# Kernel optimization log

Measured on AMD Instinct MI355X. Metric: run time of the kernel, lower is better.

Reference implementation:

```python
import jax, jax.numpy as jnp
import numpy as np

BATCH = 8192
N = 32
A_NUM = 5
EPS = 1e-10
ALPHA = jnp.array([0.01, 0.25, 0.5, 0.9, 0.99], dtype=jnp.float32)


def setup_inputs() -> dict:
    key = jax.random.key(0)
    ks = jax.random.split(key, 9)
    stdv = 1.0 / np.sqrt(N)
    u = lambda k, shape: jax.random.uniform(k, shape, jnp.float32, -stdv, stdv)
    L = N * (N - 1) // 2
    return {
        "inputs": jax.random.normal(ks[0], (BATCH, N, N), jnp.float32),
        "state": jax.random.normal(ks[1], (BATCH, A_NUM * N * N), jnp.float32),
        "WR_root": u(ks[2], (A_NUM,)),
        "Wt_root": u(ks[3], (1,)),
        "Wphi_root": u(ks[4], (1,)),
        "Ws_root": u(ks[5], (A_NUM,)),
        "Br": u(ks[6], (L, 1)),
        "Bt": u(ks[7], (L, 1)),
        "By": u(ks[8], (L, 1)),
    }


def _skew(Bvec, n):
    # Replicates the torch loop: row 0 is zeros; row k (k>=1) gets B[k-1 : 2k-1]
    # in its first k columns (overlapping slices of the flat parameter vector).
    b = Bvec.reshape(-1)
    r = jnp.arange(n)[:, None]
    c = jnp.arange(n)[None, :]
    idx = jnp.clip(r - 1 + c, 0, b.shape[0] - 1)  # B[k-1+j] for entry (k, j)
    L = jnp.where(c < r, b[idx], jnp.zeros((), b.dtype))
    return L - L.T


def _cayley(S, n):
    # MatrixExp in the source: (I - S)^{-1} (I + S)
    I = jnp.eye(n, dtype=S.dtype)
    return jnp.linalg.solve(I - S, I + S)


def _translate(A, Bvec, n):
    # M @ A @ M.T with M the Cayley 'exp' of the skew matrix built from Bvec.
    M = _cayley(_skew(Bvec, n), n)
    return jnp.einsum('ij,bjk,lk->bil', M, A, M)


def _nus(W_root, A, eps):
    # Weighted average over the a_num axis with weights W_root^2 / (sum + eps).
    W = W_root * W_root
    return jnp.einsum('a,banm->bnm', W / (W.sum() + eps), A)


def reference(inputs, state, WR_root, Wt_root, Wphi_root, Ws_root, Br, Bt, By):
    Mt_1 = state.reshape(-1, A_NUM, N, N)                 # [B, a, n, n]
    X = inputs.reshape(BATCH, N, N)                       # [B, n, n]

    Yt = _nus(WR_root, Mt_1, EPS)                         # [B, n, n]
    Rt = _translate(Yt, Br, N)

    at = (Wt_root[0] ** 2) / ((Wt_root ** 2 + Wphi_root ** 2).sum() + EPS)
    Tt = (1.0 - at) * X + at * Rt                         # Frechet mean FM
    Phit = _translate(Tt, Bt, N)

    # Per-j Frechet means, vectorized over the a_num axis.
    a = ALPHA[None, :, None, None]
    Mt = (1.0 - a) * Mt_1 + a * Phit[:, None, :, :]       # [B, a, n, n]

    St = _nus(Ws_root, Mt, EPS)
    Ot = _translate(St, By, N)                            # [B, n, n]

    return Ot, Mt.reshape(-1, A_NUM, N, N)
```

## Files before the change

### kernel.cpp

```cpp
#include <hip/hip_runtime.h>

#define NB 8192
#define ANUM 5
#define OT_ELEMS (NB * 1024)
#define EPSF 1e-10f

#define WAVE_FENCE() asm volatile("s_waitcnt lgkmcnt(0)" ::: "memory")

__global__ void cayley_kernel(const float* __restrict__ Br,
                              const float* __restrict__ Bt,
                              const float* __restrict__ By,
                              float* __restrict__ MT_out) {
  __shared__ float A[32][33];
  __shared__ float R[32][33];
  const float* B = (blockIdx.x == 0) ? Br : (blockIdx.x == 1) ? Bt : By;
  const int t = threadIdx.x;
  const int i = t >> 5, j = t & 31;
  float Lij = (j < i) ? B[i - 1 + j] : 0.0f;
  float Lji = (i < j) ? B[j - 1 + i] : 0.0f;
  float S = Lij - Lji;
  float eye = (i == j) ? 1.0f : 0.0f;
  A[i][j] = eye - S;
  R[i][j] = eye + S;
  __syncthreads();
  for (int p = 0; p < 32; ++p) {
    float f = A[i][p] / A[p][p];
    __syncthreads();
    if (i != p) {
      A[i][j] -= f * A[p][j];
      R[i][j] -= f * R[p][j];
    }
    __syncthreads();
  }
  MT_out[blockIdx.x * 1024 + j * 32 + i] = R[i][j] / A[i][i];
}

__device__ __forceinline__ void mm_MQ(const float* __restrict__ M, const float* __restrict__ buf,
                                      int i0, int j0, float acc[4][4]) {
#pragma unroll
  for (int k = 0; k < 32; ++k) {
    const float4 a = *(const float4*)(M + k * 32 + i0);
    const float4 b = *(const float4*)(buf + k * 32 + (j0 ^ (k & 28)));
    acc[0][0] = fmaf(a.x, b.x, acc[0][0]);
    acc[0][1] = fmaf(a.x, b.y, acc[0][1]);
    acc[0][2] = fmaf(a.x, b.z, acc[0][2]);
    acc[0][3] = fmaf(a.x, b.w, acc[0][3]);
    acc[1][0] = fmaf(a.y, b.x, acc[1][0]);
    acc[1][1] = fmaf(a.y, b.y, acc[1][1]);
    acc[1][2] = fmaf(a.y, b.z, acc[1][2]);
    acc[1][3] = fmaf(a.y, b.w, acc[1][3]);
    acc[2][0] = fmaf(a.z, b.x, acc[2][0]);
    acc[2][1] = fmaf(a.z, b.y, acc[2][1]);
    acc[2][2] = fmaf(a.z, b.z, acc[2][2]);
    acc[2][3] = fmaf(a.z, b.w, acc[2][3]);
    acc[3][0] = fmaf(a.w, b.x, acc[3][0]);
    acc[3][1] = fmaf(a.w, b.y, acc[3][1]);
    acc[3][2] = fmaf(a.w, b.z, acc[3][2]);
    acc[3][3] = fmaf(a.w, b.w, acc[3][3]);
  }
}

__device__ __forceinline__ void mm_PM(const float* __restrict__ buf, const float* __restrict__ M,
                                      int i0, int j0, float acc[4][4]) {
#pragma unroll
  for (int k = 0; k < 32; ++k) {
    const float4 a = *(const float4*)(buf + k * 32 + (i0 ^ (k & 28)));
    const float4 b = *(const float4*)(M + k * 32 + j0);
    acc[0][0] = fmaf(a.x, b.x, acc[0][0]);
    acc[0][1] = fmaf(a.x, b.y, acc[0][1]);
    acc[0][2] = fmaf(a.x, b.z, acc[0][2]);
    acc[0][3] = fmaf(a.x, b.w, acc[0][3]);
    acc[1][0] = fmaf(a.y, b.x, acc[1][0]);
    acc[1][1] = fmaf(a.y, b.y, acc[1][1]);
    acc[1][2] = fmaf(a.y, b.z, acc[1][2]);
    acc[1][3] = fmaf(a.y, b.w, acc[1][3]);
    acc[2][0] = fmaf(a.z, b.x, acc[2][0]);
    acc[2][1] = fmaf(a.z, b.y, acc[2][1]);
    acc[2][2] = fmaf(a.z, b.z, acc[2][2]);
    acc[2][3] = fmaf(a.z, b.w, acc[2][3]);
    acc[3][0] = fmaf(a.w, b.x, acc[3][0]);
    acc[3][1] = fmaf(a.w, b.y, acc[3][1]);
    acc[3][2] = fmaf(a.w, b.z, acc[3][2]);
    acc[3][3] = fmaf(a.w, b.w, acc[3][3]);
  }
}

__global__ __launch_bounds__(256) void spdsru_main(
    const float* __restrict__ X, const float* __restrict__ state,
    const float* __restrict__ WR, const float* __restrict__ Wt,
    const float* __restrict__ Wphi, const float* __restrict__ Ws,
    const float* __restrict__ MT, float* __restrict__ out) {
  __shared__ float sMT[3 * 1024];
  __shared__ float sBuf[4][1024];
  const int t = threadIdx.x;
  for (int idx = t; idx < 768; idx += 256)
    ((float4*)sMT)[idx] = ((const float4*)MT)[idx];

  float wr[5], wsn[5];
  float sR = 0.f, sS = 0.f;
#pragma unroll
  for (int a = 0; a < 5; ++a) { float v = WR[a]; wr[a] = v * v; sR += v * v; }
#pragma unroll
  for (int a = 0; a < 5; ++a) { float v = Ws[a]; wsn[a] = v * v; sS += v * v; }
  const float invR = 1.0f / (sR + EPSF), invS = 1.0f / (sS + EPSF);
#pragma unroll
  for (int a = 0; a < 5; ++a) { wr[a] *= invR; wsn[a] *= invS; }
  const float wt2 = Wt[0] * Wt[0], wp2 = Wphi[0] * Wphi[0];
  const float at = wt2 / (wt2 + wp2 + EPSF);
  const float omat = 1.0f - at;

  const int wave = t >> 6, lane = t & 63;
  const int i0 = (lane >> 3) << 2;
  const int j0 = (lane & 7) << 2;
  const int batch = blockIdx.x * 4 + wave;
  float* buf = sBuf[wave];
  const float* MR  = sMT;
  const float* MTt = sMT + 1024;
  const float* MY  = sMT + 2048;

  const float* stp = state + (size_t)batch * (ANUM * 1024);
  const float* xp = X + (size_t)batch * 1024;
  float4 m[5][4];
#pragma unroll
  for (int a = 0; a < 5; ++a)
#pragma unroll
    for (int r = 0; r < 4; ++r)
      m[a][r] = *(const float4*)(stp + a * 1024 + (i0 + r) * 32 + j0);
  float4 x[4];
#pragma unroll
  for (int r = 0; r < 4; ++r) x[r] = *(const float4*)(xp + (i0 + r) * 32 + j0);

  __syncthreads();

#pragma unroll
  for (int r = 0; r < 4; ++r) {
    float4 y;
    y.x = wr[0]*m[0][r].x + wr[1]*m[1][r].x + wr[2]*m[2][r].x + wr[3]*m[3][r].x + wr[4]*m[4][r].x;
    y.y = wr[0]*m[0][r].y + wr[1]*m[1][r].y + wr[2]*m[2][r].y + wr[3]*m[3][r].y + wr[4]*m[4][r].y;
    y.z = wr[0]*m[0][r].z + wr[1]*m[1][r].z + wr[2]*m[2][r].z + wr[3]*m[3][r].z + wr[4]*m[4][r].z;
    y.w = wr[0]*m[0][r].w + wr[1]*m[1][r].w + wr[2]*m[2][r].w + wr[3]*m[3][r].w + wr[4]*m[4][r].w;
    *(float4*)(buf + (i0 + r) * 32 + (j0 ^ i0)) = y;
  }
  WAVE_FENCE();

  float t1[4][4] = {};
  mm_MQ(MR, buf, i0, j0, t1);
  WAVE_FENCE();
#pragma unroll
  for (int c = 0; c < 4; ++c)
    *(float4*)(buf + (j0 + c) * 32 + (i0 ^ j0)) = make_float4(t1[0][c], t1[1][c], t1[2][c], t1[3][c]);
  WAVE_FENCE();

  float t2[4][4] = {};
  mm_PM(buf, MR, i0, j0, t2);
  WAVE_FENCE();
#pragma unroll
  for (int r = 0; r < 4; ++r) {
    float4 v;
    v.x = omat * x[r].x + at * t2[r][0];
    v.y = omat * x[r].y + at * t2[r][1];
    v.z = omat * x[r].z + at * t2[r][2];
    v.w = omat * x[r].w + at * t2[r][3];
    *(float4*)(buf + (i0 + r) * 32 + (j0 ^ i0)) = v;
  }
  WAVE_FENCE();

  float u1[4][4] = {};
  mm_MQ(MTt, buf, i0, j0, u1);
  WAVE_FENCE();
#pragma unroll
  for (int c = 0; c < 4; ++c)
    *(float4*)(buf + (j0 + c) * 32 + (i0 ^ j0)) = make_float4(u1[0][c], u1[1][c], u1[2][c], u1[3][c]);
  WAVE_FENCE();

  float u2[4][4] = {};
  mm_PM(buf, MTt, i0, j0, u2);
  WAVE_FENCE();

  float* outMt = out + OT_ELEMS + (size_t)batch * (ANUM * 1024);
  float4 stl[4];
#pragma unroll
  for (int r = 0; r < 4; ++r) stl[r] = make_float4(0.f, 0.f, 0.f, 0.f);
  const float alpha[5] = {0.01f, 0.25f, 0.5f, 0.9f, 0.99f};
#pragma unroll
  for (int a = 0; a < 5; ++a) {
    const float al = alpha[a], om = 1.0f - al;
#pragma unroll
    for (int r = 0; r < 4; ++r) {
      float4 v;
      v.x = om * m[a][r].x + al * u2[r][0];
      v.y = om * m[a][r].y + al * u2[r][1];
      v.z = om * m[a][r].z + al * u2[r][2];
      v.w = om * m[a][r].w + al * u2[r][3];
      *(float4*)(outMt + a * 1024 + (i0 + r) * 32 + j0) = v;
      stl[r].x = fmaf(wsn[a], v.x, stl[r].x);
      stl[r].y = fmaf(wsn[a], v.y, stl[r].y);
      stl[r].z = fmaf(wsn[a], v.z, stl[r].z);
      stl[r].w = fmaf(wsn[a], v.w, stl[r].w);
    }
  }
#pragma unroll
  for (int r = 0; r < 4; ++r)
    *(float4*)(buf + (i0 + r) * 32 + (j0 ^ i0)) = stl[r];
  WAVE_FENCE();

  float v1[4][4] = {};
  mm_MQ(MY, buf, i0, j0, v1);
  WAVE_FENCE();
#pragma unroll
  for (int c = 0; c < 4; ++c)
    *(float4*)(buf + (j0 + c) * 32 + (i0 ^ j0)) = make_float4(v1[0][c], v1[1][c], v1[2][c], v1[3][c]);
  WAVE_FENCE();

  float v2[4][4] = {};
  mm_PM(buf, MY, i0, j0, v2);
  float* outOt = out + (size_t)batch * 1024;
#pragma unroll
  for (int r = 0; r < 4; ++r)
    *(float4*)(outOt + (i0 + r) * 32 + j0) = make_float4(v2[r][0], v2[r][1], v2[r][2], v2[r][3]);
}

extern "C" void kernel_launch(void* const* d_in, const int* in_sizes, int n_in,
                              void* d_out, int out_size, void* d_ws, size_t ws_size,
                              hipStream_t stream) {
  const float* X     = (const float*)d_in[0];
  const float* state = (const float*)d_in[1];
  const float* WR    = (const float*)d_in[2];
  const float* Wt    = (const float*)d_in[3];
  const float* Wphi  = (const float*)d_in[4];
  const float* Ws    = (const float*)d_in[5];
  const float* Br    = (const float*)d_in[6];
  const float* Bt    = (const float*)d_in[7];
  const float* By    = (const float*)d_in[8];
  float* mt_ws = (float*)d_ws;
  float* outp = (float*)d_out;

  cayley_kernel<<<3, 1024, 0, stream>>>(Br, Bt, By, mt_ws);
  spdsru_main<<<NB / 4, 256, 0, stream>>>(X, state, WR, Wt, Wphi, Ws, mt_ws, outp);
}
```

Measured before the change: 108.1 us.

## Fold state into two accumulators and reload state to cut register pressure

Instead of keeping all 80 state floats in registers across the six matmuls, the kernel reduces the state once into two weighted sums: U for the WR mix and V for the (1-alpha)-weighted Ws mix. St is then rebuilt algebraically as V + cP*Phit, and the state is reloaded from global memory (likely from cache) when writing Mt. The launch-bounds hint now asks for 4 blocks per CU. The aim is lower VGPR use and higher occupancy, at the cost of a second read of state and a small change in floating-point rounding order.

```diff
diff --git a/kernel.cpp b/kernel.cpp
--- a/kernel.cpp
+++ b/kernel.cpp
@@ -85,26 +85,35 @@
   }
 }
 
-__global__ __launch_bounds__(256) void spdsru_main(
+__global__ __launch_bounds__(256, 4) void spdsru_main(
     const float* __restrict__ X, const float* __restrict__ state,
     const float* __restrict__ WR, const float* __restrict__ Wt,
     const float* __restrict__ Wphi, const float* __restrict__ Ws,
-    const float* __restrict__ MT, float* __restrict__ out) {
-  __shared__ float sMT[3 * 1024];
+    const float* __restrict__ Mws, float* __restrict__ out) {
+  __shared__ float sM[3 * 1024];
   __shared__ float sBuf[4][1024];
   const int t = threadIdx.x;
   for (int idx = t; idx < 768; idx += 256)
-    ((float4*)sMT)[idx] = ((const float4*)MT)[idx];
-
-  float wr[5], wsn[5];
-  float sR = 0.f, sS = 0.f;
-#pragma unroll
-  for (int a = 0; a < 5; ++a) { float v = WR[a]; wr[a] = v * v; sR += v * v; }
-#pragma unroll
-  for (int a = 0; a < 5; ++a) { float v = Ws[a]; wsn[a] = v * v; sS += v * v; }
-  const float invR = 1.0f / (sR + EPSF), invS = 1.0f / (sS + EPSF);
-#pragma unroll
-  for (int a = 0; a < 5; ++a) { wr[a] *= invR; wsn[a] *= invS; }
+    ((float4*)sM)[idx] = ((const float4*)Mws)[idx];
+
+  const float alpha[5] = {0.01f, 0.25f, 0.5f, 0.9f, 0.99f};
+  float wr[5], va[5];
+  float cP = 0.f;
+  {
+    float sR = 0.f, sS = 0.f, wq[5];
+#pragma unroll
+    for (int a = 0; a < 5; ++a) { float v = WR[a]; wr[a] = v * v; sR += v * v; }
+#pragma unroll
+    for (int a = 0; a < 5; ++a) { float v = Ws[a]; wq[a] = v * v; sS += v * v; }
+    const float invR = 1.0f / (sR + EPSF), invS = 1.0f / (sS + EPSF);
+#pragma unroll
+    for (int a = 0; a < 5; ++a) {
+      wr[a] *= invR;
+      float w = wq[a] * invS;
+      va[a] = w * (1.0f - alpha[a]);
+      cP += w * alpha[a];
+    }
+  }
   const float wt2 = Wt[0] * Wt[0], wp2 = Wphi[0] * Wphi[0];
   const float at = wt2 / (wt2 + wp2 + EPSF);
   const float omat = 1.0f - at;
@@ -114,45 +123,48 @@
   const int j0 = (lane & 7) << 2;
   const int batch = blockIdx.x * 4 + wave;
   float* buf = sBuf[wave];
-  const float* MR  = sMT;
-  const float* MTt = sMT + 1024;
-  const float* MY  = sMT + 2048;
+  const float* MRb = sM;
+  const float* MTb = sM + 1024;
+  const float* MYb = sM + 2048;
+
+  const float* xp = X + (size_t)batch * 1024;
+  float4 x[4];
+#pragma unroll
+  for (int r = 0; r < 4; ++r) x[r] = *(const float4*)(xp + (i0 + r) * 32 + j0);
 
   const float* stp = state + (size_t)batch * (ANUM * 1024);
-  const float* xp = X + (size_t)batch * 1024;
-  float4 m[5][4];
-#pragma unroll
-  for (int a = 0; a < 5; ++a)
-#pragma unroll
-    for (int r = 0; r < 4; ++r)
-      m[a][r] = *(const float4*)(stp + a * 1024 + (i0 + r) * 32 + j0);
-  float4 x[4];
-#pragma unroll
-  for (int r = 0; r < 4; ++r) x[r] = *(const float4*)(xp + (i0 + r) * 32 + j0);
+  float4 U[4], V[4];
+#pragma unroll
+  for (int r = 0; r < 4; ++r) { U[r] = make_float4(0.f, 0.f, 0.f, 0.f); V[r] = U[r]; }
+#pragma unroll
+  for (int a = 0; a < 5; ++a) {
+#pragma unroll
+    for (int r = 0; r < 4; ++r) {
+      const float4 v = *(const float4*)(stp + a * 1024 + (i0 + r) * 32 + j0);
+      U[r].x = fmaf(wr[a], v.x, U[r].x);  V[r].x = fmaf(va[a], v.x, V[r].x);
+      U[r].y = fmaf(wr[a], v.y, U[r].y);  V[r].y = fmaf(va[a], v.y, V[r].y);
+      U[r].z = fmaf(wr[a], v.z, U[r].z);  V[r].z = fmaf(va[a], v.z, V[r].z);
+      U[r].w = fmaf(wr[a], v.w, U[r].w);  V[r].w = fmaf(va[a], v.w, V[r].w);
+    }
+  }
 
   __syncthreads();
 
 #pragma unroll
-  for (int r = 0; r < 4; ++r) {
-    float4 y;
-    y.x = wr[0]*m[0][r].x + wr[1]*m[1][r].x + wr[2]*m[2][r].x + wr[3]*m[3][r].x + wr[4]*m[4][r].x;
-    y.y = wr[0]*m[0][r].y + wr[1]*m[1][r].y + wr[2]*m[2][r].y + wr[3]*m[3][r].y + wr[4]*m[4][r].y;
-    y.z = wr[0]*m[0][r].z + wr[1]*m[1][r].z + wr[2]*m[2][r].z + wr[3]*m[3][r].z + wr[4]*m[4][r].z;
-    y.w = wr[0]*m[0][r].w + wr[1]*m[1][r].w + wr[2]*m[2][r].w + wr[3]*m[3][r].w + wr[4]*m[4][r].w;
-    *(float4*)(buf + (i0 + r) * 32 + (j0 ^ i0)) = y;
-  }
-  WAVE_FENCE();
-
-  float t1[4][4] = {};
-  mm_MQ(MR, buf, i0, j0, t1);
+  for (int r = 0; r < 4; ++r)
+    *(float4*)(buf + (i0 + r) * 32 + (j0 ^ i0)) = U[r];
+  WAVE_FENCE();
+
+  float g[4][4] = {};
+  mm_MQ(MRb, buf, i0, j0, g);
   WAVE_FENCE();
 #pragma unroll
   for (int c = 0; c < 4; ++c)
-    *(float4*)(buf + (j0 + c) * 32 + (i0 ^ j0)) = make_float4(t1[0][c], t1[1][c], t1[2][c], t1[3][c]);
+    *(float4*)(buf + (j0 + c) * 32 + (i0 ^ j0)) = make_float4(g[0][c], g[1][c], g[2][c], g[3][c]);
   WAVE_FENCE();
 
   float t2[4][4] = {};
-  mm_PM(buf, MR, i0, j0, t2);
+  mm_PM(buf, MRb, i0, j0, t2);
   WAVE_FENCE();
 #pragma unroll
   for (int r = 0; r < 4; ++r) {
@@ -166,7 +178,7 @@
   WAVE_FENCE();
 
   float u1[4][4] = {};
-  mm_MQ(MTt, buf, i0, j0, u1);
+  mm_MQ(MTb, buf, i0, j0, u1);
   WAVE_FENCE();
 #pragma unroll
   for (int c = 0; c < 4; ++c)
@@ -174,50 +186,49 @@
   WAVE_FENCE();
 
   float u2[4][4] = {};
-  mm_PM(buf, MTt, i0, j0, u2);
+  mm_PM(buf, MTb, i0, j0, u2);
   WAVE_FENCE();
 
   float* outMt = out + OT_ELEMS + (size_t)batch * (ANUM * 1024);
-  float4 stl[4];
-#pragma unroll
-  for (int r = 0; r < 4; ++r) stl[r] = make_float4(0.f, 0.f, 0.f, 0.f);
-  const float alpha[5] = {0.01f, 0.25f, 0.5f, 0.9f, 0.99f};
 #pragma unroll
   for (int a = 0; a < 5; ++a) {
     const float al = alpha[a], om = 1.0f - al;
 #pragma unroll
     for (int r = 0; r < 4; ++r) {
-      float4 v;
-      v.x = om * m[a][r].x + al * u2[r][0];
-      v.y = om * m[a][r].y + al * u2[r][1];
-      v.z = om * m[a][r].z + al * u2[r][2];
-      v.w = om * m[a][r].w + al * u2[r][3];
-      *(float4*)(outMt + a * 1024 + (i0 + r) * 32 + j0) = v;
-      stl[r].x = fmaf(wsn[a], v.x, stl[r].x);
-      stl[r].y = fmaf(wsn[a], v.y, stl[r].y);
-      stl[r].z = fmaf(wsn[a], v.z, stl[r].z);
-      stl[r].w = fmaf(wsn[a], v.w, stl[r].w);
-    }
-  }
-#pragma unroll
-  for (int r = 0; r < 4; ++r)
-    *(float4*)(buf + (i0 + r) * 32 + (j0 ^ i0)) = stl[r];
+      const float4 v = *(const float4*)(stp + a * 1024 + (i0 + r) * 32 + j0);
+      float4 w;
+      w.x = om * v.x + al * u2[r][0];
+      w.y = om * v.y + al * u2[r][1];
+      w.z = om * v.z + al * u2[r][2];
+      w.w = om * v.w + al * u2[r][3];
+      *(float4*)(outMt + a * 1024 + (i0 + r) * 32 + j0) = w;
+    }
+  }
+#pragma unroll
+  for (int r = 0; r < 4; ++r) {
+    float4 s;
+    s.x = fmaf(cP, u2[r][0], V[r].x);
+    s.y = fmaf(cP, u2[r][1], V[r].y);
+    s.z = fmaf(cP, u2[r][2], V[r].z);
+    s.w = fmaf(cP, u2[r][3], V[r].w);
+    *(float4*)(buf + (i0 + r) * 32 + (j0 ^ i0)) = s;
+  }
   WAVE_FENCE();
 
   float v1[4][4] = {};
-  mm_MQ(MY, buf, i0, j0, v1);
+  mm_MQ(MYb, buf, i0, j0, v1);
   WAVE_FENCE();
 #pragma unroll
   for (int c = 0; c < 4; ++c)
     *(float4*)(buf + (j0 + c) * 32 + (i0 ^ j0)) = make_float4(v1[0][c], v1[1][c], v1[2][c], v1[3][c]);
   WAVE_FENCE();
 
-  float v2[4][4] = {};
-  mm_PM(buf, MY, i0, j0, v2);
+  float o[4][4] = {};
+  mm_PM(buf, MYb, i0, j0, o);
   float* outOt = out + (size_t)batch * 1024;
 #pragma unroll
   for (int r = 0; r < 4; ++r)
-    *(float4*)(outOt + (i0 + r) * 32 + j0) = make_float4(v2[r][0], v2[r][1], v2[r][2], v2[r][3]);
+    *(float4*)(outOt + (i0 + r) * 32 + j0) = make_float4(o[r][0], o[r][1], o[r][2], o[r][3]);
 }
 
 extern "C" void kernel_launch(void* const* d_in, const int* in_sizes, int n_in,
```

Measured after the change: 171.1 us. +58.3%, slower.
